# Optimization experiments

Hardware: AMD Instinct MI355X
Metric: run time of the kernel (lower is better)

## Reference

```python
import jax, jax.numpy as jnp
import numpy as np

NEG_BIG = -9e15

def setup_inputs() -> dict:
    key = jax.random.key(0)
    k1, k2, k3, k4 = jax.random.split(key, 4)
    N, Fin, Fout = 8192, 256, 128
    x = jax.random.normal(k1, (N, Fin), dtype=jnp.float32)
    adj = jax.random.randint(k2, (N, N), 0, 2, dtype=jnp.int32)
    # xavier-uniform-like init
    limW = float(np.sqrt(6.0 / (Fin + Fout)))
    W = jax.random.uniform(k3, (Fin, Fout), minval=-limW, maxval=limW, dtype=jnp.float32)
    lima = float(np.sqrt(6.0 / (2 * Fout + 1)))
    a = jax.random.uniform(k4, (2 * Fout, 1), minval=-lima, maxval=lima, dtype=jnp.float32)
    return {"x": x, "adj": adj, "W": W, "a": a}

def reference(x, adj, W, a, alpha=0.2):
    # h: (N, Fout)
    h = x @ W
    Fout = W.shape[1]
    # Split a into source/target halves: e[i,j] = leakyrelu(h_i·a1 + h_j·a2)
    a1, a2 = a[:Fout, 0], a[Fout:, 0]
    s = h @ a1  # (N,) row (source) scores
    t = h @ a2  # (N,) col (target) scores
    e = jax.nn.leaky_relu(s[:, None] + t[None, :], negative_slope=alpha)  # (N, N)
    e = jnp.where(adj > 0, e, NEG_BIG)
    attention = jax.nn.softmax(e, axis=1)
    # dropout omitted (eval mode / training=False)
    return attention @ h
```

## Files before the change

kernel.cpp:

```cpp
#include <hip/hip_runtime.h>
#include <hip/hip_bf16.h>

typedef __attribute__((ext_vector_type(8))) short short8;
typedef __attribute__((ext_vector_type(4))) short short4v;
typedef __attribute__((ext_vector_type(4))) float f32x4;

typedef const __attribute__((address_space(1))) unsigned gcu32;
typedef __attribute__((address_space(3))) unsigned lu32;

#define NR 8192
#define LOG2E 1.4426950408889634f

__device__ __forceinline__ short f2bf(float f) {
  return __builtin_bit_cast(short, __float2bfloat16(f));
}

__global__ __launch_bounds__(256) void k_gemm_h(const float* __restrict__ x,
                                                const float* __restrict__ W,
                                                const float* __restrict__ a,
                                                short* __restrict__ HT2,
                                                float* __restrict__ sv,
                                                float* __restrict__ tv) {
  __shared__ short WT[128][136];
  const int tid = threadIdx.x;
  const int w = tid >> 6;
  const int L = tid & 63;
  const int lm = L & 15;
  const int q = L >> 4;
  const int i0 = blockIdx.x * 64;

  f32x4 acc[8];
#pragma unroll
  for (int nn = 0; nn < 8; ++nn) acc[nn] = (f32x4){0.f, 0.f, 0.f, 0.f};

  for (int kc = 0; kc < 256; kc += 128) {
    if (kc) __syncthreads();
#pragma unroll
    for (int p = 0; p < 16; ++p) {
      int idx = p * 256 + tid;
      int k = idx >> 5;
      int f4 = (idx & 31) * 4;
      float4 v = *(const float4*)&W[(kc + k) * 128 + f4];
      WT[f4 + 0][k] = f2bf(v.x);
      WT[f4 + 1][k] = f2bf(v.y);
      WT[f4 + 2][k] = f2bf(v.z);
      WT[f4 + 3][k] = f2bf(v.w);
    }
    __syncthreads();
#pragma unroll
    for (int ks = 0; ks < 4; ++ks) {
      int row = i0 + 16 * w + lm;
      const float* xp = &x[(size_t)row * 256 + kc + ks * 32 + q * 8];
      float4 xa = *(const float4*)xp;
      float4 xb = *(const float4*)(xp + 4);
      short8 af;
      af[0] = f2bf(xa.x); af[1] = f2bf(xa.y); af[2] = f2bf(xa.z); af[3] = f2bf(xa.w);
      af[4] = f2bf(xb.x); af[5] = f2bf(xb.y); af[6] = f2bf(xb.z); af[7] = f2bf(xb.w);
#pragma unroll
      for (int nn = 0; nn < 8; ++nn) {
        short8 bf = *(const short8*)&WT[nn * 16 + lm][ks * 32 + q * 8];
        acc[nn] = __builtin_amdgcn_mfma_f32_16x16x32_bf16(af, bf, acc[nn], 0, 0, 0);
      }
    }
  }

  const int ib = i0 + 16 * w + 4 * q;
  const int tbase = (ib >> 5) * 4096 + (ib & 31);
  float a1v[8], a2v[8];
#pragma unroll
  for (int nn = 0; nn < 8; ++nn) {
    a1v[nn] = a[nn * 16 + lm];
    a2v[nn] = a[128 + nn * 16 + lm];
  }
  float sr[4] = {0.f, 0.f, 0.f, 0.f};
  float tr[4] = {0.f, 0.f, 0.f, 0.f};
#pragma unroll
  for (int nn = 0; nn < 8; ++nn) {
    int f = nn * 16 + lm;
    short4v o;
    o[0] = f2bf(acc[nn][0]);
    o[1] = f2bf(acc[nn][1]);
    o[2] = f2bf(acc[nn][2]);
    o[3] = f2bf(acc[nn][3]);
    *(short4v*)&HT2[tbase + f * 32] = o;
#pragma unroll
    for (int r = 0; r < 4; ++r) {
      sr[r] += acc[nn][r] * a1v[nn];
      tr[r] += acc[nn][r] * a2v[nn];
    }
  }
#pragma unroll
  for (int d = 1; d < 16; d <<= 1) {
#pragma unroll
    for (int r = 0; r < 4; ++r) {
      sr[r] += __shfl_xor(sr[r], d);
      tr[r] += __shfl_xor(tr[r], d);
    }
  }
  if (lm == 0) {
#pragma unroll
    for (int r = 0; r < 4; ++r) {
      sv[ib + r] = sr[r] * LOG2E;
      tv[ib + r] = tr[r] * LOG2E;
    }
  }
}

__global__ __launch_bounds__(512, 4) void k_flash(const int* __restrict__ adj,
                                                  const short* __restrict__ HT2,
                                                  const float* __restrict__ sv,
                                                  const float* __restrict__ tv,
                                                  float* __restrict__ part,
                                                  float* __restrict__ lpart) {
  __shared__ short lds_s[32768];
  unsigned* ldsw = (unsigned*)lds_s;
  const int tid = threadIdx.x;
  const int w = tid >> 6;
  const int L = tid & 63;
  const int lm = L & 15;
  const int q = L >> 4;
  const int sp = blockIdx.x & 15;
  const int it = blockIdx.x >> 4;
  const int i0 = it * 128;

  const int row0 = i0 + 16 * w + lm;
  const float s0 = sv[row0];
  const size_t ar0 = (size_t)row0 * NR;

  const int ksrc = (tid & 0x1FC) | ((tid & 3) ^ ((tid >> 3) & 3));

  f32x4 acc[8];
#pragma unroll
  for (int nn = 0; nn < 8; ++nn) acc[nn] = (f32x4){0.f, 0.f, 0.f, 0.f};
  float l0 = 0.f;

  const int tile0 = sp * 16;
  int jb = tile0 * 32 + q * 8;
  int4 sa00 = *(const int4*)&adj[ar0 + jb];
  int4 sa01 = *(const int4*)&adj[ar0 + jb + 4];

  for (int t = 0; t < 16; ++t) {
    if ((t & 7) == 0) {
      __syncthreads();
      const short* gs = &HT2[(size_t)(tile0 + t) * 4096 + ksrc * 8];
#pragma unroll
      for (int z = 0; z < 8; ++z)
        __builtin_amdgcn_global_load_lds((gcu32*)(gs + z * 4096),
                                         (lu32*)&ldsw[z * 2048 + w * 256], 16, 0, 0);
      __syncthreads();
    }
    int4 a00 = sa00, a01 = sa01;
    if (t + 1 < 16) {
      int jn = (tile0 + t + 1) * 32 + q * 8;
      sa00 = *(const int4*)&adj[ar0 + jn];
      sa01 = *(const int4*)&adj[ar0 + jn + 4];
    }
    const int jc = (tile0 + t) * 32 + q * 8;
    float4 tv0 = *(const float4*)&tv[jc];
    float4 tv1 = *(const float4*)&tv[jc + 4];
    const int tt = t & 7;
    short8 bf[8];
#pragma unroll
    for (int nn = 0; nn < 8; ++nn) {
      int f = nn * 16 + lm;
      bf[nn] = *(const short8*)&ldsw[tt * 2048 + f * 16 + ((q ^ ((f >> 1) & 3)) * 4)];
    }

    int av0[8] = {a00.x, a00.y, a00.z, a00.w, a01.x, a01.y, a01.z, a01.w};
    float tvl[8] = {tv0.x, tv0.y, tv0.z, tv0.w, tv1.x, tv1.y, tv1.z, tv1.w};
    short8 p0;
#pragma unroll
    for (int e = 0; e < 8; ++e) {
      float v0 = s0 + tvl[e];
      float e0 = fmaxf(v0, 0.2f * v0);
      float pp0 = (av0[e] > 0) ? __builtin_amdgcn_exp2f(e0) : 0.f;
      l0 += pp0;
      p0[e] = f2bf(pp0);
    }
#pragma unroll
    for (int nn = 0; nn < 8; ++nn)
      acc[nn] = __builtin_amdgcn_mfma_f32_16x16x32_bf16(p0, bf[nn], acc[nn], 0, 0, 0);
  }
  __syncthreads();

  float* my = (float*)lds_s + w * 2048;
#pragma unroll
  for (int nn = 0; nn < 8; ++nn)
#pragma unroll
    for (int r = 0; r < 4; ++r)
      my[(4 * q + r) * 128 + nn * 16 + lm] = acc[nn][r];
  float* pbase = part + ((size_t)sp * NR + i0 + 16 * w) * 128;
#pragma unroll
  for (int c = 0; c < 8; ++c) {
    int idx = (c * 64 + L) * 4;
    *(float4*)&pbase[idx] = *(const float4*)&my[idx];
  }

  l0 += __shfl_xor(l0, 16);
  l0 += __shfl_xor(l0, 32);
  if (q == 0) lpart[sp * NR + row0] = l0;
}

__global__ __launch_bounds__(256) void k_reduce(const float* __restrict__ part,
                                                const float* __restrict__ lpart,
                                                float* __restrict__ out, int S) {
  int idx4 = blockIdx.x * 256 + threadIdx.x;
  int idx = idx4 * 4;
  int i = idx >> 7;
  float4 sum = {0.f, 0.f, 0.f, 0.f};
  for (int sp = 0; sp < S; ++sp) {
    float4 v = *(const float4*)&part[(size_t)sp * (NR * 128) + idx];
    sum.x += v.x; sum.y += v.y; sum.z += v.z; sum.w += v.w;
  }
  float l = 0.f;
  for (int sp = 0; sp < S; ++sp) l += lpart[sp * NR + i];
  float inv = (l > 0.f) ? 1.f / l : 0.f;
  float4 o = {sum.x * inv, sum.y * inv, sum.z * inv, sum.w * inv};
  *(float4*)&out[idx] = o;
}

extern "C" void kernel_launch(void* const* d_in, const int* in_sizes, int n_in,
                              void* d_out, int out_size, void* d_ws, size_t ws_size,
                              hipStream_t stream) {
  const float* x = (const float*)d_in[0];
  const int* adj = (const int*)d_in[1];
  const float* W = (const float*)d_in[2];
  const float* a = (const float*)d_in[3];
  float* out = (float*)d_out;

  char* ws = (char*)d_ws;
  short* HT2 = (short*)(ws + 0);
  float* sv = (float*)(ws + 2097152);
  float* tv = (float*)(ws + 2129920);
  float* lpart = (float*)(ws + 2162688);
  float* part = (float*)(ws + 2719744);

  const int S = 16;

  hipLaunchKernelGGL(k_gemm_h, dim3(128), dim3(256), 0, stream, x, W, a, HT2, sv, tv);
  hipLaunchKernelGGL(k_flash, dim3(64 * S), dim3(512), 0, stream, adj, HT2, sv, tv,
                     part, lpart);
  hipLaunchKernelGGL(k_reduce, dim3((NR * 128) / 1024), dim3(256), 0, stream, part,
                     lpart, out, S);
}
```

Baseline: 419.0 us.

## Store split-K partials as bf16 and double flash block rows to 256

The flash kernel now uses 1024-thread blocks covering 256 rows, so each HT tile loaded into LDS is shared by twice as many rows. The upper and lower halves of the block cooperatively load alternating tiles. Partial accumulators are written as bf16 instead of fp32 and converted back in the reduce kernel, halving partial write and read traffic. The cost is extra rounding error in the partial sums before the final 16-way reduction. Larger blocks may also cut occupancy.

```diff
diff --git a/kernel.cpp b/kernel.cpp
--- a/kernel.cpp
+++ b/kernel.cpp
@@ -13,6 +13,9 @@
 
 __device__ __forceinline__ short f2bf(float f) {
   return __builtin_bit_cast(short, __float2bfloat16(f));
+}
+__device__ __forceinline__ float bf2f(short s) {
+  return __builtin_bit_cast(float, ((unsigned)(unsigned short)s) << 16);
 }
 
 __global__ __launch_bounds__(256) void k_gemm_h(const float* __restrict__ x,
@@ -106,12 +109,12 @@
   }
 }
 
-__global__ __launch_bounds__(512, 4) void k_flash(const int* __restrict__ adj,
-                                                  const short* __restrict__ HT2,
-                                                  const float* __restrict__ sv,
-                                                  const float* __restrict__ tv,
-                                                  float* __restrict__ part,
-                                                  float* __restrict__ lpart) {
+__global__ __launch_bounds__(1024, 4) void k_flash(const int* __restrict__ adj,
+                                                   const short* __restrict__ HT2,
+                                                   const float* __restrict__ sv,
+                                                   const float* __restrict__ tv,
+                                                   short* __restrict__ part,
+                                                   float* __restrict__ lpart) {
   __shared__ short lds_s[32768];
   unsigned* ldsw = (unsigned*)lds_s;
   const int tid = threadIdx.x;
@@ -121,13 +124,15 @@
   const int q = L >> 4;
   const int sp = blockIdx.x & 15;
   const int it = blockIdx.x >> 4;
-  const int i0 = it * 128;
+  const int i0 = it * 256;
 
   const int row0 = i0 + 16 * w + lm;
   const float s0 = sv[row0];
   const size_t ar0 = (size_t)row0 * NR;
 
-  const int ksrc = (tid & 0x1FC) | ((tid & 3) ^ ((tid >> 3) & 3));
+  const int c511 = tid & 511;
+  const int ksrc = (c511 & 0x1FC) | ((c511 & 3) ^ ((c511 >> 3) & 3));
+  const int hi = tid >> 9;
 
   f32x4 acc[8];
 #pragma unroll
@@ -142,11 +147,11 @@
   for (int t = 0; t < 16; ++t) {
     if ((t & 7) == 0) {
       __syncthreads();
-      const short* gs = &HT2[(size_t)(tile0 + t) * 4096 + ksrc * 8];
-#pragma unroll
-      for (int z = 0; z < 8; ++z)
-        __builtin_amdgcn_global_load_lds((gcu32*)(gs + z * 4096),
-                                         (lu32*)&ldsw[z * 2048 + w * 256], 16, 0, 0);
+      const short* gs = &HT2[(size_t)(tile0 + t + hi) * 4096 + ksrc * 8];
+#pragma unroll
+      for (int z = 0; z < 4; ++z)
+        __builtin_amdgcn_global_load_lds((gcu32*)(gs + z * 2 * 4096),
+                                         (lu32*)&ldsw[z * 4096 + w * 256], 16, 0, 0);
       __syncthreads();
     }
     int4 a00 = sa00, a01 = sa01;
@@ -183,17 +188,17 @@
   }
   __syncthreads();
 
-  float* my = (float*)lds_s + w * 2048;
+  short* my = lds_s + w * 2048;
 #pragma unroll
   for (int nn = 0; nn < 8; ++nn)
 #pragma unroll
     for (int r = 0; r < 4; ++r)
-      my[(4 * q + r) * 128 + nn * 16 + lm] = acc[nn][r];
-  float* pbase = part + ((size_t)sp * NR + i0 + 16 * w) * 128;
-#pragma unroll
-  for (int c = 0; c < 8; ++c) {
-    int idx = (c * 64 + L) * 4;
-    *(float4*)&pbase[idx] = *(const float4*)&my[idx];
+      my[(4 * q + r) * 128 + nn * 16 + lm] = f2bf(acc[nn][r]);
+  short* pb = part + ((size_t)sp * NR + i0 + 16 * w) * 128;
+#pragma unroll
+  for (int c = 0; c < 4; ++c) {
+    int idx = (c * 64 + L) * 8;
+    *(uint4*)&pb[idx] = *(const uint4*)&my[idx];
   }
 
   l0 += __shfl_xor(l0, 16);
@@ -201,7 +206,7 @@
   if (q == 0) lpart[sp * NR + row0] = l0;
 }
 
-__global__ __launch_bounds__(256) void k_reduce(const float* __restrict__ part,
+__global__ __launch_bounds__(256) void k_reduce(const short* __restrict__ part,
                                                 const float* __restrict__ lpart,
                                                 float* __restrict__ out, int S) {
   int idx4 = blockIdx.x * 256 + threadIdx.x;
@@ -209,8 +214,9 @@
   int i = idx >> 7;
   float4 sum = {0.f, 0.f, 0.f, 0.f};
   for (int sp = 0; sp < S; ++sp) {
-    float4 v = *(const float4*)&part[(size_t)sp * (NR * 128) + idx];
-    sum.x += v.x; sum.y += v.y; sum.z += v.z; sum.w += v.w;
+    short4v v = *(const short4v*)&part[(size_t)sp * (NR * 128) + idx];
+    sum.x += bf2f(v[0]); sum.y += bf2f(v[1]);
+    sum.z += bf2f(v[2]); sum.w += bf2f(v[3]);
   }
   float l = 0.f;
   for (int sp = 0; sp < S; ++sp) l += lpart[sp * NR + i];
@@ -233,12 +239,12 @@
   float* sv = (float*)(ws + 2097152);
   float* tv = (float*)(ws + 2129920);
   float* lpart = (float*)(ws + 2162688);
-  float* part = (float*)(ws + 2719744);
+  short* part = (short*)(ws + 2719744);
 
   const int S = 16;
 
   hipLaunchKernelGGL(k_gemm_h, dim3(128), dim3(256), 0, stream, x, W, a, HT2, sv, tv);
-  hipLaunchKernelGGL(k_flash, dim3(64 * S), dim3(512), 0, stream, adj, HT2, sv, tv,
+  hipLaunchKernelGGL(k_flash, dim3(32 * S), dim3(1024), 0, stream, adj, HT2, sv, tv,
                      part, lpart);
   hipLaunchKernelGGL(k_reduce, dim3((NR * 128) / 1024), dim3(256), 0, stream, part,
                      lpart, out, S);
```

Measured after the change: 415.7 us. No clear change (-0.8%).
